# Kernel optimization log

Measured on AMD Instinct MI355X. Metric: run time of the kernel, lower is better.

The kernel has to match this reference:

```python
import jax, jax.numpy as jnp
import numpy as np
from jax import lax

B = 64      # batch (n_image == n_caption)
R = 36      # image regions
W = 32      # words per caption (uniform cap_lens)
D = 1024    # embedding dim
LAMBDA_SOFTMAX = 9.0
LAMBDA_LSE = 6.0
ALPHA = 0.1
MARGIN = 0.2
OT_ITER = 20
BETA = 0.5
EPS = 1e-8


def setup_inputs() -> dict:
    key = jax.random.key(0)
    k1, k2, k3 = jax.random.split(key, 3)
    im = jax.random.normal(k1, (B, R, D), jnp.float32)
    s = jax.random.normal(k2, (B, W, D), jnp.float32)
    x = jax.random.normal(k3, (B, W, D), jnp.float32)
    s_l = jnp.full((B,), W, dtype=jnp.int32)
    return {"im": im, "s": s, "s_l": s_l, "x": x}


def _l2norm(a, axis):
    # matches torch l2norm: x / (sqrt(sum(x^2)) + eps)
    return a / (jnp.sqrt(jnp.sum(a * a, axis=axis, keepdims=True)) + EPS)


def _scores_t2i(im, s, x):
    # ---- func_attention (t2i): query = caption words, context = image regions ----
    # raw attn: (c, i, r, w) = context @ query^T for every caption/image pair
    attn = jnp.einsum('ird,cwd->cirw', im, s)
    attn = jax.nn.leaky_relu(attn, negative_slope=0.1)   # clipped_l2norm
    attn = _l2norm(attn, axis=3)                          # l2norm over query (word) axis
    attn = jnp.swapaxes(attn, 2, 3)                       # (c, i, w, r)
    attn = jax.nn.softmax(attn * LAMBDA_SOFTMAX, axis=3)  # softmax over regions
    wctx = jnp.einsum('ciwr,ird->ciwd', attn, im)         # weighted context (c,i,w,d)

    # cosine similarity between caption words and weighted context, over d
    num = jnp.einsum('cwd,ciwd->ciw', s, wctx)
    w1 = jnp.linalg.norm(s, axis=2)[:, None, :]           # (c,1,w)
    w2 = jnp.linalg.norm(wctx, axis=3)                    # (c,i,w)
    row_sim = num / jnp.maximum(w1 * w2, EPS)             # (c,i,w)

    # LogSumExp aggregation over words
    sim = jax.nn.logsumexp(row_sim * LAMBDA_LSE, axis=2) / LAMBDA_LSE  # (c,i)

    # ---- OT cost matrix: cosine distance between x words and image regions ----
    xn = x / (jnp.linalg.norm(x, axis=2, keepdims=True) + 1e-12)
    imn = im / (jnp.linalg.norm(im, axis=2, keepdims=True) + 1e-12)
    C = 1.0 - jnp.einsum('cwd,ird->ciwr', xn, imn)        # (c,i,W,R)

    # ---- IPOT (uniform marginals, beta=0.5, one inner step) ----
    A = jnp.exp(-C / BETA)
    T0 = jnp.ones_like(C)
    sigma0 = jnp.full(C.shape[:2] + (R,), 1.0 / R, dtype=C.dtype)

    def body(carry, _):
        T, sigma = carry
        Q = A * T                                          # (c,i,W,R)
        delta = 1.0 / (W * jnp.einsum('ciwr,cir->ciw', Q, sigma))
        sigma = 1.0 / (R * jnp.einsum('ciwr,ciw->cir', Q, delta))
        T = delta[..., :, None] * Q * sigma[..., None, :]
        return (T, sigma), None

    (T, _), _ = lax.scan(body, (T0, sigma0), None, length=OT_ITER)
    ot_dist = jnp.sum(C * T, axis=(-2, -1))               # trace(C^T T) -> (c,i)
    ot_sim = -ot_dist

    # torch code concatenates per-caption columns: scores[img, cap]
    return sim.T, ot_sim.T                                 # (n_img, n_cap)


def reference(im, s, s_l, x):
    # s_l is uniform (== W); the per-caption slicing in the torch loop is a no-op.
    scores, scores_ot = _scores_t2i(im, s, x)
    n = scores.shape[0]

    diag = jnp.diagonal(scores)
    diag_ot = jnp.diagonal(scores_ot)

    cost_s = jnp.maximum(MARGIN + scores - diag[:, None], 0.0)
    cost_im = jnp.maximum(MARGIN + scores - diag[None, :], 0.0)
    cost_s_ot = jnp.maximum(MARGIN + scores_ot - diag_ot[:, None], 0.0)
    cost_im_ot = jnp.maximum(MARGIN + scores_ot - diag_ot[None, :], 0.0)

    off = 1.0 - jnp.eye(n, dtype=scores.dtype)
    cost_s = cost_s * off
    cost_im = cost_im * off
    cost_s_ot = cost_s_ot * off
    cost_im_ot = cost_im_ot * off

    cost_s = cost_s + ALPHA * cost_s_ot
    cost_im = cost_im + ALPHA * cost_im_ot

    # max_violation = True
    cost_s = jnp.max(cost_s, axis=1)
    cost_im = jnp.max(cost_im, axis=0)
    cost_s_ot = jnp.max(cost_s_ot, axis=1)
    cost_im_ot = jnp.max(cost_im_ot, axis=0)

    return (jnp.sum(cost_s) + jnp.sum(cost_im),
            jnp.sum(cost_s_ot) + jnp.sum(cost_im_ot))
```

## Files before the change

kernel.cpp:

```cpp
#include <hip/hip_runtime.h>
#include <cstdint>
#include <cstddef>


typedef __attribute__((ext_vector_type(8))) short short8;
typedef __attribute__((ext_vector_type(4))) float f32x4;
typedef __attribute__((ext_vector_type(2))) float f2;

__device__ __forceinline__ unsigned short f2bf(float f) {
  unsigned u = __float_as_uint(f);
  u += 0x7FFFu + ((u >> 16) & 1u);
  return (unsigned short)(u >> 16);
}
__device__ __forceinline__ float rcpf(float x) { return __builtin_amdgcn_rcpf(x); }

__global__ __launch_bounds__(256) void k_prep(const float* __restrict__ s,
                                              const float* __restrict__ x,
                                              const float* __restrict__ im,
                                              unsigned short* __restrict__ Ab,
                                              unsigned short* __restrict__ Bb,
                                              float* __restrict__ w1,
                                              float* __restrict__ xn_r,
                                              float* __restrict__ imn_r,
                                              float* __restrict__ G) {
  int blk = blockIdx.x;
  if (blk < 2304) {
    int b = blk / 36, r = blk - b * 36;
    int wid = threadIdx.x >> 6, l = threadIdx.x & 63;
    const float* rowr = im + ((size_t)b*36 + r) * 1024;
    float4 my[4];
    #pragma unroll
    for (int j = 0; j < 4; ++j) my[j] = ((const float4*)rowr)[j*64 + l];
    float* Gr = G + ((size_t)b*36 + r) * 36;
    for (int rp = wid; rp < 36; rp += 4) {
      const float* rowp = im + ((size_t)b*36 + rp) * 1024;
      float p = 0.f;
      #pragma unroll
      for (int j = 0; j < 4; ++j) {
        float4 u = ((const float4*)rowp)[j*64 + l];
        p += my[j].x*u.x + my[j].y*u.y + my[j].z*u.z + my[j].w*u.w;
      }
      #pragma unroll
      for (int o = 32; o > 0; o >>= 1) p += __shfl_down(p, o, 64);
      if (l == 0) Gr[rp] = p;
    }
    return;
  }
  int row = blk - 2304, tid = threadIdx.x;
  const float* src; unsigned short* dst; float* np; int recip;
  if (row < 2048)      { src = s  + (size_t)row * 1024;          dst = Ab + (size_t)row * 1024;          np = w1    + row;          recip = 0; }
  else if (row < 4096) { src = x  + (size_t)(row - 2048) * 1024; dst = Ab + (size_t)row * 1024;          np = xn_r  + (row - 2048); recip = 1; }
  else                 { src = im + (size_t)(row - 4096) * 1024; dst = Bb + (size_t)(row - 4096) * 1024; np = imn_r + (row - 4096); recip = 1; }
  float4 f = ((const float4*)src)[tid];
  ushort4 h;
  h.x = f2bf(f.x); h.y = f2bf(f.y); h.z = f2bf(f.z); h.w = f2bf(f.w);
  ((ushort4*)dst)[tid] = h;
  float p = f.x*f.x + f.y*f.y + f.z*f.z + f.w*f.w;
  #pragma unroll
  for (int o = 32; o > 0; o >>= 1) p += __shfl_down(p, o, 64);
  __shared__ float red[4];
  if ((tid & 63) == 0) red[tid >> 6] = p;
  __syncthreads();
  if (tid == 0) {
    float n = sqrtf(red[0] + red[1] + red[2] + red[3]);
    *np = recip ? 1.f / (n + 1e-12f) : n;
  }
}

__global__ __launch_bounds__(256) void k_gemm_mfma(const unsigned short* __restrict__ A,
                                                   const unsigned short* __restrict__ B,
                                                   unsigned short* __restrict__ dot) {
  __shared__ unsigned short lA[128 * 32];
  __shared__ unsigned short lB[96 * 32];
  int tid = threadIdx.x;
  int bn = blockIdx.x * 96, bm = blockIdx.y * 128;
  int wid = tid >> 6, l = tid & 63;
  int wr = (wid >> 1) * 64, wc = (wid & 1) * 48;
  int lr = l & 15, lq = l >> 4;

  f32x4 acc[4][3] = {};

  int row_a = tid >> 2;
  int kq = (tid & 3) * 8;
  const unsigned short* gA = A + (size_t)(bm + row_a) * 1024 + kq;
  const unsigned short* gB = B + (size_t)(bn + row_a) * 1024 + kq;
  unsigned loff = (unsigned)tid * 16u;

  for (int kt = 0; kt < 1024; kt += 32) {
    __builtin_amdgcn_global_load_lds(
        (const __attribute__((address_space(1))) void*)(gA + kt),
        (__attribute__((address_space(3))) void*)((char*)lA + loff), 16, 0, 0);
    __builtin_amdgcn_global_load_lds(
        (const __attribute__((address_space(1))) void*)(gA + 64*1024 + kt),
        (__attribute__((address_space(3))) void*)((char*)lA + 4096 + loff), 16, 0, 0);
    __builtin_amdgcn_global_load_lds(
        (const __attribute__((address_space(1))) void*)(gB + kt),
        (__attribute__((address_space(3))) void*)((char*)lB + loff), 16, 0, 0);
    if (tid < 128)
      __builtin_amdgcn_global_load_lds(
          (const __attribute__((address_space(1))) void*)(gB + 64*1024 + kt),
          (__attribute__((address_space(3))) void*)((char*)lB + 4096 + loff), 16, 0, 0);
    __syncthreads();

    short8 af[4], bfr[3];
    #pragma unroll
    for (int mi = 0; mi < 4; ++mi)
      af[mi] = *(const short8*)&lA[(wr + mi*16 + lr) * 32 + lq * 8];
    #pragma unroll
    for (int ni = 0; ni < 3; ++ni)
      bfr[ni] = *(const short8*)&lB[(wc + ni*16 + lr) * 32 + lq * 8];
    #pragma unroll
    for (int mi = 0; mi < 4; ++mi)
      #pragma unroll
      for (int ni = 0; ni < 3; ++ni)
        acc[mi][ni] = __builtin_amdgcn_mfma_f32_16x16x32_bf16(af[mi], bfr[ni], acc[mi][ni], 0, 0, 0);
    __syncthreads();
  }

  #pragma unroll
  for (int mi = 0; mi < 4; ++mi)
    #pragma unroll
    for (int ni = 0; ni < 3; ++ni) {
      int gcol = bn + wc + ni*16 + lr;
      #pragma unroll
      for (int q = 0; q < 4; ++q) {
        int grow = bm + wr + mi*16 + lq*4 + q;
        dot[(size_t)grow * 2304 + gcol] = f2bf(acc[mi][ni][q]);
      }
    }
}

template<int C>
__device__ __forceinline__ float dpp_add(float v) {
  return v + __int_as_float(__builtin_amdgcn_mov_dpp(__float_as_int(v), C, 0xF, 0xF, true));
}
template<int C>
__device__ __forceinline__ float dpp_max(float v) {
  return fmaxf(v, __int_as_float(__builtin_amdgcn_mov_dpp(__float_as_int(v), C, 0xF, 0xF, true)));
}
__device__ __forceinline__ float bsum32(float v) {
  v = dpp_add<0xB1>(v);
  v = dpp_add<0x4E>(v);
  v = dpp_add<0x141>(v);
  v = dpp_add<0x128>(v);
  v += __shfl_xor(v, 16, 64);
  return v;
}
__device__ __forceinline__ float bmax32(float v) {
  v = dpp_max<0xB1>(v);
  v = dpp_max<0x4E>(v);
  v = dpp_max<0x141>(v);
  v = dpp_max<0x128>(v);
  v = fmaxf(v, __shfl_xor(v, 16, 64));
  return v;
}

__global__ __launch_bounds__(256, 4) void k_pair2(const unsigned short* __restrict__ dotb,
                                                  const float* __restrict__ Gm,
                                                  const float* __restrict__ w1m,
                                                  const float* __restrict__ xnrm,
                                                  const float* __restrict__ imnrm,
                                                  float* __restrict__ S,
                                                  float* __restrict__ Sot) {
  int wid  = threadIdx.x >> 6;
  int g    = blockIdx.x * 4 + wid;
  int pair = g >> 1;
  int role = g & 1;
  int c = pair >> 6, i = pair & 63;
  int l = threadIdx.x & 63;
  int h = l >> 5, w = l & 31;
  int r0 = h * 18;

  if (role == 0) {
    const unsigned* drow = (const unsigned*)(dotb + (size_t)(c*32 + w) * 2304 + i*36 + r0);
    float w1 = w1m[c*32 + w];

    f2 d2[9];
    #pragma unroll
    for (int k = 0; k < 9; ++k) {
      unsigned u = drow[k];
      d2[k][0] = __uint_as_float(u << 16);
      d2[k][1] = __uint_as_float(u & 0xFFFF0000u);
    }

    f2 p2[9];
    #pragma unroll
    for (int k = 0; k < 9; ++k) {
      f2 t = d2[k] * 0.1f;
      f2 fv;
      fv[0] = fmaxf(d2[k][0], t[0]);
      fv[1] = fmaxf(d2[k][1], t[1]);
      f2 sq = fv * fv;
      float t0 = bsum32(sq[0]);
      float t1 = bsum32(sq[1]);
      f2 rs;
      rs[0] = __builtin_amdgcn_rsqf(fmaxf(t0 * 0.012345679f, 1e-30f));
      rs[1] = __builtin_amdgcn_rsqf(fmaxf(t1 * 0.012345679f, 1e-30f));
      p2[k] = fv * rs;
    }
    float mx = fmaxf(fmaxf(p2[0][0], p2[0][1]), fmaxf(p2[1][0], p2[1][1]));
    #pragma unroll
    for (int k = 2; k < 9; ++k) mx = fmaxf(mx, fmaxf(p2[k][0], p2[k][1]));
    mx = fmaxf(mx, __shfl_xor(mx, 32, 64));

    f2 e2[9];
    f2 sum2 = {0.f, 0.f}, nu2 = {0.f, 0.f};
    #pragma unroll
    for (int k = 0; k < 9; ++k) {
      e2[k][0] = __expf(p2[k][0] - mx);
      e2[k][1] = __expf(p2[k][1] - mx);
      sum2 += e2[k];
      nu2 += e2[k] * d2[k];
    }
    float sum = sum2[0] + sum2[1];
    float numu = nu2[0] + nu2[1];
    sum  += __shfl_xor(sum, 32, 64);
    numu += __shfl_xor(numu, 32, 64);
    float inv = rcpf(sum);
    float num = numu * inv;

    f2 afull[18];
    #pragma unroll
    for (int k = 0; k < 9; ++k) {
      f2 a = e2[k] * inv;
      f2 o;
      o[0] = __shfl_xor(a[0], 32, 64);
      o[1] = __shfl_xor(a[1], 32, 64);
      afull[k][0]     = h ? o[0] : a[0];
      afull[k][1]     = h ? o[1] : a[1];
      afull[9 + k][0] = h ? a[0] : o[0];
      afull[9 + k][1] = h ? a[1] : o[1];
    }

    int iu = __builtin_amdgcn_readfirstlane(i);
    const float* Gi = Gm + (size_t)iu * 1296;
    float w2sq = 0.f;
    #pragma unroll 4
    for (int rp = 0; rp < 36; ++rp) {
      const f2* Gr = (const f2*)(Gi + rp * 36);
      f2 in2 = {0.f, 0.f};
      #pragma unroll
      for (int q = 0; q < 18; ++q) in2 += Gr[q] * afull[q];
      float ar = (rp & 1) ? afull[rp >> 1][1] : afull[rp >> 1][0];
      w2sq = fmaf(ar, in2[0] + in2[1], w2sq);
    }
    float w2 = __builtin_amdgcn_sqrtf(w2sq);
    float rs6 = 6.f * num * rcpf(fmaxf(w1 * w2, 1e-8f));

    float mw = bmax32(rs6);
    float se = bsum32(__expf(rs6 - mw));
    float sim = (mw + __logf(se)) * (1.f / 6.f);
    if (l == 0) S[i*64 + c] = sim;
  } else {
    const unsigned* xrow = (const unsigned*)(dotb + (size_t)(2048 + c*32 + w) * 2304 + i*36 + r0);
    float xnr = xnrm[c*32 + w];

    f2 Cm2[9];
    const f2* ir = (const f2*)(imnrm + i*36 + r0);
    #pragma unroll
    for (int k = 0; k < 9; ++k) {
      unsigned u = xrow[k];
      f2 xv;
      xv[0] = __uint_as_float(u << 16);
      xv[1] = __uint_as_float(u & 0xFFFF0000u);
      xv *= xnr;
      Cm2[k] = 1.f - xv * ir[k];
    }

    f2 Am2[9], Qm2[9], sg2[9];
    #pragma unroll
    for (int k = 0; k < 9; ++k) {
      Am2[k][0] = __expf(-2.f * Cm2[k][0]);
      Am2[k][1] = __expf(-2.f * Cm2[k][1]);
      Qm2[k] = Am2[k];
      sg2[k] = (f2){1.f/36.f, 1.f/36.f};
    }
    float delta = 0.f;
    for (int it = 0; it < 20; ++it) {
      f2 t2 = {0.f, 0.f};
      #pragma unroll
      for (int k = 0; k < 9; ++k) t2 += Qm2[k] * sg2[k];
      float tt = t2[0] + t2[1];
      tt += __shfl_xor(tt, 32, 64);
      delta = rcpf(32.f * tt);
      #pragma unroll
      for (int k = 0; k < 9; ++k) {
        f2 qd = Qm2[k] * delta;
        float q0 = bsum32(qd[0]);
        float q1 = bsum32(qd[1]);
        sg2[k][0] = rcpf(36.f * q0);
        sg2[k][1] = rcpf(36.f * q1);
      }
      if (it < 19) {
        #pragma unroll
        for (int k = 0; k < 9; ++k) Qm2[k] = (Am2[k] * delta) * Qm2[k] * sg2[k];
      }
    }
    f2 ot2 = {0.f, 0.f};
    #pragma unroll
    for (int k = 0; k < 9; ++k) ot2 += Cm2[k] * (Qm2[k] * delta * sg2[k]);
    float ot = ot2[0] + ot2[1];
    ot += __shfl_xor(ot, 32, 64);
    ot = bsum32(ot);
    if (l == 0) Sot[i*64 + c] = -ot;
  }
}

__global__ __launch_bounds__(256) void k_reduce(const float* __restrict__ Sg,
                                                const float* __restrict__ Sotg,
                                                float* __restrict__ outp) {
  __shared__ float s[4096];
  __shared__ float so[4096];
  __shared__ float red0[256], red1[256];
  int tid = threadIdx.x;
  for (int e = tid; e < 4096; e += 256) { s[e] = Sg[e]; so[e] = Sotg[e]; }
  __syncthreads();
  float m0 = 0.f, m1 = 0.f;
  if (tid < 64) {
    int i = tid;
    float di = s[i*65], dio = so[i*65];
    for (int c2 = 0; c2 < 64; ++c2) {
      if (c2 == i) continue;
      float cs  = fmaxf(0.2f + s[i*64 + c2]  - di,  0.f);
      float cso = fmaxf(0.2f + so[i*64 + c2] - dio, 0.f);
      m0 = fmaxf(m0, cs + 0.1f * cso);
      m1 = fmaxf(m1, cso);
    }
  } else if (tid < 128) {
    int c2 = tid - 64;
    float dc = s[c2*65], dco = so[c2*65];
    for (int i = 0; i < 64; ++i) {
      if (i == c2) continue;
      float cim  = fmaxf(0.2f + s[i*64 + c2]  - dc,  0.f);
      float cimo = fmaxf(0.2f + so[i*64 + c2] - dco, 0.f);
      m0 = fmaxf(m0, cim + 0.1f * cimo);
      m1 = fmaxf(m1, cimo);
    }
  }
  red0[tid] = m0; red1[tid] = m1;
  __syncthreads();
  if (tid == 0) {
    float a0 = 0.f, a1 = 0.f;
    for (int t = 0; t < 128; ++t) { a0 += red0[t]; a1 += red1[t]; }
    outp[0] = a0;
    outp[1] = a1;
  }
}

extern "C" void kernel_launch(void* const* d_in, const int* in_sizes, int n_in,
                              void* d_out, int out_size, void* d_ws, size_t ws_size,
                              hipStream_t stream) {
  (void)in_sizes; (void)n_in; (void)out_size; (void)ws_size;
  const float* im = (const float*)d_in[0];
  const float* s  = (const float*)d_in[1];
  const float* x  = (const float*)d_in[3];
  float* out = (float*)d_out;

  unsigned short* Ab   = (unsigned short*)d_ws;
  unsigned short* Bb   = Ab + (size_t)4096 * 1024;
  unsigned short* dotb = Bb + (size_t)2304 * 1024;
  float* G     = (float*)(dotb + (size_t)4096 * 2304);
  float* w1    = G + 64*36*36;
  float* xn_r  = w1 + 2048;
  float* imn_r = xn_r + 2048;
  float* S     = imn_r + 2304;
  float* Sot   = S + 4096;

  k_prep<<<dim3(8704), 256, 0, stream>>>(s, x, im, Ab, Bb, w1, xn_r, imn_r, G);
  k_gemm_mfma<<<dim3(24, 32), 256, 0, stream>>>(Ab, Bb, dotb);
  k_pair2<<<dim3(2048), 256, 0, stream>>>(dotb, G, w1, xn_r, imn_r, S, Sot);
  k_reduce<<<dim3(1), 256, 0, stream>>>(S, Sot, out);
}
```

Before: 115.1 us.

## Compute per-image region Gram matrices inside the bf16 MFMA GEMM kernel

Drops the 2304 scalar fp32 Gram-matrix blocks from the prep kernel and adds 36 extra blocks to the MFMA GEMM launch. These reuse the bf16 image rows as both operands and keep only the same-image 36x36 entries of each 128x192 tile. The aim is to replace the dot-product-plus-shuffle Gram work with tensor-core tiles inside an existing launch. In exchange, G is now computed from bf16-rounded inputs instead of fp32, and the last tiles read past the end of the B buffer into the following workspace; those extra values are masked before being written.

Result: slower. 119.9 us (+4.2%).

```diff
diff --git a/kernel.cpp b/kernel.cpp
--- a/kernel.cpp
+++ b/kernel.cpp
@@ -21,32 +21,8 @@
                                               unsigned short* __restrict__ Bb,
                                               float* __restrict__ w1,
                                               float* __restrict__ xn_r,
-                                              float* __restrict__ imn_r,
-                                              float* __restrict__ G) {
-  int blk = blockIdx.x;
-  if (blk < 2304) {
-    int b = blk / 36, r = blk - b * 36;
-    int wid = threadIdx.x >> 6, l = threadIdx.x & 63;
-    const float* rowr = im + ((size_t)b*36 + r) * 1024;
-    float4 my[4];
-    #pragma unroll
-    for (int j = 0; j < 4; ++j) my[j] = ((const float4*)rowr)[j*64 + l];
-    float* Gr = G + ((size_t)b*36 + r) * 36;
-    for (int rp = wid; rp < 36; rp += 4) {
-      const float* rowp = im + ((size_t)b*36 + rp) * 1024;
-      float p = 0.f;
-      #pragma unroll
-      for (int j = 0; j < 4; ++j) {
-        float4 u = ((const float4*)rowp)[j*64 + l];
-        p += my[j].x*u.x + my[j].y*u.y + my[j].z*u.z + my[j].w*u.w;
-      }
-      #pragma unroll
-      for (int o = 32; o > 0; o >>= 1) p += __shfl_down(p, o, 64);
-      if (l == 0) Gr[rp] = p;
-    }
-    return;
-  }
-  int row = blk - 2304, tid = threadIdx.x;
+                                              float* __restrict__ imn_r) {
+  int row = blockIdx.x, tid = threadIdx.x;
   const float* src; unsigned short* dst; float* np; int recip;
   if (row < 2048)      { src = s  + (size_t)row * 1024;          dst = Ab + (size_t)row * 1024;          np = w1    + row;          recip = 0; }
   else if (row < 4096) { src = x  + (size_t)(row - 2048) * 1024; dst = Ab + (size_t)row * 1024;          np = xn_r  + (row - 2048); recip = 1; }
@@ -69,20 +45,34 @@
 
 __global__ __launch_bounds__(256) void k_gemm_mfma(const unsigned short* __restrict__ A,
                                                    const unsigned short* __restrict__ B,
-                                                   unsigned short* __restrict__ dot) {
+                                                   unsigned short* __restrict__ dot,
+                                                   float* __restrict__ G) {
   __shared__ unsigned short lA[128 * 32];
   __shared__ unsigned short lB[96 * 32];
+  int gb = (int)blockIdx.x;
   int tid = threadIdx.x;
-  int bn = blockIdx.x * 96, bm = blockIdx.y * 128;
   int wid = tid >> 6, l = tid & 63;
   int wr = (wid >> 1) * 64, wc = (wid & 1) * 48;
   int lr = l & 15, lq = l >> 4;
 
+  bool gram = gb >= 768;
+  int bm, bn;
+  const unsigned short* baseA;
+  if (!gram) {
+    bn = (gb % 24) * 96; bm = (gb / 24) * 128;
+    baseA = A;
+  } else {
+    int t = gb - 768;
+    bm = (t >> 1) * 128;
+    bn = (bm / 36) * 36 + (t & 1) * 96;
+    baseA = B;
+  }
+
   f32x4 acc[4][3] = {};
 
   int row_a = tid >> 2;
   int kq = (tid & 3) * 8;
-  const unsigned short* gA = A + (size_t)(bm + row_a) * 1024 + kq;
+  const unsigned short* gA = baseA + (size_t)(bm + row_a) * 1024 + kq;
   const unsigned short* gB = B + (size_t)(bn + row_a) * 1024 + kq;
   unsigned loff = (unsigned)tid * 16u;
 
@@ -117,17 +107,35 @@
     __syncthreads();
   }
 
-  #pragma unroll
-  for (int mi = 0; mi < 4; ++mi)
-    #pragma unroll
-    for (int ni = 0; ni < 3; ++ni) {
-      int gcol = bn + wc + ni*16 + lr;
-      #pragma unroll
-      for (int q = 0; q < 4; ++q) {
-        int grow = bm + wr + mi*16 + lq*4 + q;
-        dot[(size_t)grow * 2304 + gcol] = f2bf(acc[mi][ni][q]);
+  if (!gram) {
+    #pragma unroll
+    for (int mi = 0; mi < 4; ++mi)
+      #pragma unroll
+      for (int ni = 0; ni < 3; ++ni) {
+        int gcol = bn + wc + ni*16 + lr;
+        #pragma unroll
+        for (int q = 0; q < 4; ++q) {
+          int grow = bm + wr + mi*16 + lq*4 + q;
+          dot[(size_t)grow * 2304 + gcol] = f2bf(acc[mi][ni][q]);
+        }
       }
-    }
+  } else {
+    #pragma unroll
+    for (int mi = 0; mi < 4; ++mi)
+      #pragma unroll
+      for (int ni = 0; ni < 3; ++ni) {
+        int q_im = bn + wc + ni*16 + lr;
+        #pragma unroll
+        for (int q = 0; q < 4; ++q) {
+          int p_im = bm + wr + mi*16 + lq*4 + q;
+          if (q_im < 2304) {
+            int bp = p_im / 36, bq = q_im / 36;
+            if (bp == bq)
+              G[((size_t)bp*36 + (p_im - bp*36)) * 36 + (q_im - bq*36)] = acc[mi][ni][q];
+          }
+        }
+      }
+  }
 }
 
 template<int C>
@@ -366,8 +374,8 @@
   float* S     = imn_r + 2304;
   float* Sot   = S + 4096;
 
-  k_prep<<<dim3(8704), 256, 0, stream>>>(s, x, im, Ab, Bb, w1, xn_r, imn_r, G);
-  k_gemm_mfma<<<dim3(24, 32), 256, 0, stream>>>(Ab, Bb, dotb);
+  k_prep<<<dim3(6400), 256, 0, stream>>>(s, x, im, Ab, Bb, w1, xn_r, imn_r);
+  k_gemm_mfma<<<dim3(804), 256, 0, stream>>>(Ab, Bb, dotb, G);
   k_pair2<<<dim3(2048), 256, 0, stream>>>(dotb, G, w1, xn_r, imn_r, S, Sot);
   k_reduce<<<dim3(1), 256, 0, stream>>>(S, Sot, out);
 }
```

## Remap OT wave lanes so word reductions use DPP-only 16-lane sums

Applied to the files above, without the earlier changes.

The IPOT half of the pair kernel now maps each lane to two words (w and w+16) and a strided set of regions, instead of one word and 18 contiguous regions. The per-region column sum over words then becomes an in-lane add plus a 16-lane DPP reduction, dropping the cross-row shuffle that each of the 18 bsum32 calls per iteration needed. The per-word row sum now takes two shuffle rounds per component instead of one. The aim is fewer LDS-backed shuffles in the 20-iteration loop, at the cost of strided, less coalesced loads of the x-dot rows and norms.

Result: faster. 101.7 us, median of 2 (-11.6%).

```diff
diff --git a/kernel.cpp b/kernel.cpp
--- a/kernel.cpp
+++ b/kernel.cpp
@@ -146,6 +146,13 @@
   v += __shfl_xor(v, 16, 64);
   return v;
 }
+__device__ __forceinline__ float bsum16(float v) {
+  v = dpp_add<0xB1>(v);
+  v = dpp_add<0x4E>(v);
+  v = dpp_add<0x141>(v);
+  v = dpp_add<0x128>(v);
+  return v;
+}
 __device__ __forceinline__ float bmax32(float v) {
   v = dpp_max<0xB1>(v);
   v = dpp_max<0x4E>(v);
@@ -168,10 +175,10 @@
   int role = g & 1;
   int c = pair >> 6, i = pair & 63;
   int l = threadIdx.x & 63;
-  int h = l >> 5, w = l & 31;
-  int r0 = h * 18;
 
   if (role == 0) {
+    int h = l >> 5, w = l & 31;
+    int r0 = h * 18;
     const unsigned* drow = (const unsigned*)(dotb + (size_t)(c*32 + w) * 2304 + i*36 + r0);
     float w1 = w1m[c*32 + w];
 
@@ -252,56 +259,65 @@
     float sim = (mw + __logf(se)) * (1.f / 6.f);
     if (l == 0) S[i*64 + c] = sim;
   } else {
-    const unsigned* xrow = (const unsigned*)(dotb + (size_t)(2048 + c*32 + w) * 2304 + i*36 + r0);
-    float xnr = xnrm[c*32 + w];
+    int rq = l >> 4, w16 = l & 15;
+    int dsel = rq >> 1;
+    bool hi = (rq & 1);
+    const unsigned* xrow0 = (const unsigned*)(dotb + (size_t)(2048 + c*32 + w16) * 2304 + i*36);
+    const unsigned* xrow1 = (const unsigned*)(dotb + (size_t)(2048 + c*32 + w16 + 16) * 2304 + i*36);
+    float xnr0 = xnrm[c*32 + w16];
+    float xnr1 = xnrm[c*32 + w16 + 16];
 
     f2 Cm2[9];
-    const f2* ir = (const f2*)(imnrm + i*36 + r0);
-    #pragma unroll
-    for (int k = 0; k < 9; ++k) {
-      unsigned u = xrow[k];
+    #pragma unroll
+    for (int m = 0; m < 9; ++m) {
+      unsigned u0 = xrow0[2*m + dsel];
+      unsigned u1 = xrow1[2*m + dsel];
+      float xv0 = __uint_as_float(hi ? (u0 & 0xFFFF0000u) : (u0 << 16));
+      float xv1 = __uint_as_float(hi ? (u1 & 0xFFFF0000u) : (u1 << 16));
+      float inr = imnrm[i*36 + 4*m + rq];
       f2 xv;
-      xv[0] = __uint_as_float(u << 16);
-      xv[1] = __uint_as_float(u & 0xFFFF0000u);
-      xv *= xnr;
-      Cm2[k] = 1.f - xv * ir[k];
-    }
-
-    f2 Am2[9], Qm2[9], sg2[9];
-    #pragma unroll
-    for (int k = 0; k < 9; ++k) {
-      Am2[k][0] = __expf(-2.f * Cm2[k][0]);
-      Am2[k][1] = __expf(-2.f * Cm2[k][1]);
-      Qm2[k] = Am2[k];
-      sg2[k] = (f2){1.f/36.f, 1.f/36.f};
-    }
-    float delta = 0.f;
+      xv[0] = xv0 * xnr0;
+      xv[1] = xv1 * xnr1;
+      Cm2[m] = 1.f - xv * inr;
+    }
+
+    f2 Am2[9], Qm2[9];
+    float sg[9];
+    #pragma unroll
+    for (int m = 0; m < 9; ++m) {
+      Am2[m][0] = __expf(-2.f * Cm2[m][0]);
+      Am2[m][1] = __expf(-2.f * Cm2[m][1]);
+      Qm2[m] = Am2[m];
+      sg[m] = 1.f / 36.f;
+    }
+    f2 delta = {0.f, 0.f};
     for (int it = 0; it < 20; ++it) {
       f2 t2 = {0.f, 0.f};
       #pragma unroll
-      for (int k = 0; k < 9; ++k) t2 += Qm2[k] * sg2[k];
-      float tt = t2[0] + t2[1];
-      tt += __shfl_xor(tt, 32, 64);
-      delta = rcpf(32.f * tt);
-      #pragma unroll
-      for (int k = 0; k < 9; ++k) {
-        f2 qd = Qm2[k] * delta;
-        float q0 = bsum32(qd[0]);
-        float q1 = bsum32(qd[1]);
-        sg2[k][0] = rcpf(36.f * q0);
-        sg2[k][1] = rcpf(36.f * q1);
+      for (int m = 0; m < 9; ++m) t2 += Qm2[m] * sg[m];
+      t2[0] += __shfl_xor(t2[0], 16, 64);
+      t2[1] += __shfl_xor(t2[1], 16, 64);
+      t2[0] += __shfl_xor(t2[0], 32, 64);
+      t2[1] += __shfl_xor(t2[1], 32, 64);
+      delta[0] = rcpf(32.f * t2[0]);
+      delta[1] = rcpf(32.f * t2[1]);
+      #pragma unroll
+      for (int m = 0; m < 9; ++m) {
+        f2 qd = Qm2[m] * delta;
+        float q = bsum16(qd[0] + qd[1]);
+        sg[m] = rcpf(36.f * q);
       }
       if (it < 19) {
         #pragma unroll
-        for (int k = 0; k < 9; ++k) Qm2[k] = (Am2[k] * delta) * Qm2[k] * sg2[k];
+        for (int m = 0; m < 9; ++m) Qm2[m] = (Am2[m] * delta) * Qm2[m] * sg[m];
       }
     }
     f2 ot2 = {0.f, 0.f};
     #pragma unroll
-    for (int k = 0; k < 9; ++k) ot2 += Cm2[k] * (Qm2[k] * delta * sg2[k]);
-    float ot = ot2[0] + ot2[1];
+    for (int m = 0; m < 9; ++m) ot2 += Cm2[m] * (Qm2[m] * delta * sg[m]);
+    float ot = bsum16(ot2[0] + ot2[1]);
+    ot += __shfl_xor(ot, 16, 64);
     ot += __shfl_xor(ot, 32, 64);
-    ot = bsum32(ot);
     if (l == 0) Sot[i*64 + c] = -ot;
   }
 }
```
